# Kernel optimization log

Measured on AMD Instinct MI355X. Metric: run time of the kernel, lower is better.

Reference implementation:

```python
import jax, jax.numpy as jnp
import numpy as np

S, I, CM, C, D, CZ = 128, 512, 256, 32, 32, 128
EPS = 1e-5


def setup_inputs() -> dict:
    key = jax.random.key(0)
    ks = jax.random.split(key, 7)
    x = jax.random.normal(ks[0], (1, S, I, CM), dtype=jnp.float32)
    norm_w = 1.0 + 0.1 * jax.random.normal(ks[1], (CM,), dtype=jnp.float32)
    norm_b = 0.1 * jax.random.normal(ks[2], (CM,), dtype=jnp.float32)
    Wa = jax.random.normal(ks[3], (C, CM), dtype=jnp.float32) / np.sqrt(CM)
    Wb = jax.random.normal(ks[4], (D, CM), dtype=jnp.float32) / np.sqrt(CM)
    Wo = jax.random.normal(ks[5], (CZ, C * D), dtype=jnp.float32) / np.sqrt(C * D)
    bo = 0.1 * jax.random.normal(ks[6], (CZ,), dtype=jnp.float32)
    return {"x": x, "norm_w": norm_w, "norm_b": norm_b, "Wa": Wa, "Wb": Wb, "Wo": Wo, "bo": bo}


def reference(x, norm_w, norm_b, Wa, Wb, Wo, bo):
    m = x[0]                                   # [S, I, CM] (drop leading batch dim)
    mu = jnp.mean(m, axis=-1, keepdims=True)
    var = jnp.mean((m - mu) ** 2, axis=-1, keepdims=True)
    ln = (m - mu) * jax.lax.rsqrt(var + EPS) * norm_w + norm_b
    a = jnp.einsum('sim,cm->sic', ln, Wa)      # [S, I, C]
    b = jnp.einsum('sjm,dm->sjd', ln, Wb)      # [S, J, D]
    s = a.shape[0]
    # outer product mean over S: [I, J, C, D]; flatten order is (c, d) -> c*D + d,
    # matching the reshape(chunk, C, J, D) -> permute(0,2,1,3) -> flatten in the original.
    o = jnp.einsum('sic,sjd->ijcd', a, b) * (1.0 / s)
    z = o.reshape(o.shape[0], o.shape[1], C * D) @ Wo.T + bo  # [I, J, CZ]
    return z[None]                             # [1, I, J, CZ]
```

## Files before the change

kernel.cpp:

```cpp
#include <hip/hip_runtime.h>

#define EPS 1e-5f

typedef _Float16 half8 __attribute__((ext_vector_type(8)));
typedef _Float16 half4 __attribute__((ext_vector_type(4)));
typedef float f32x4 __attribute__((ext_vector_type(4)));

#define AB_STRIDE 72
#define AB_CHUNK  (16384 * AB_STRIDE)

__device__ __forceinline__ void load16_to_lds(const void* g, void* l) {
    __builtin_amdgcn_global_load_lds((__attribute__((address_space(1))) void*)g,
                                     (__attribute__((address_space(3))) void*)l, 16, 0, 0);
}

__global__ void k_cvt(const float* __restrict__ Wo, const float* __restrict__ Wa,
                      const float* __restrict__ Wb, _Float16* __restrict__ WoH,
                      _Float16* __restrict__ WabH)
{
    int t = blockIdx.x * 256 + threadIdx.x;
    if (t < 32768) {
        int n  = t >> 8;
        int k4 = (t & 255) * 4;
        float4 v = *(const float4*)(Wo + (size_t)n * 1024 + k4);
        int c = k4 >> 5, d0 = k4 & 31;
        _Float16* dst = WoH + (size_t)n * 1024 + c;
        dst[(d0 + 0) * 32] = (_Float16)v.x;
        dst[(d0 + 1) * 32] = (_Float16)v.y;
        dst[(d0 + 2) * 32] = (_Float16)v.z;
        dst[(d0 + 3) * 32] = (_Float16)v.w;
    } else {
        int idx = (t - 32768) * 4;
        const float* src = (idx < 8192) ? (Wa + idx) : (Wb + (idx - 8192));
        float4 v = *(const float4*)src;
        half4 h;
        h[0] = (_Float16)v.x; h[1] = (_Float16)v.y; h[2] = (_Float16)v.z; h[3] = (_Float16)v.w;
        *(half4*)(WabH + idx) = h;
    }
}

__global__ __launch_bounds__(512, 4)
void k1_ln_proj(const float* __restrict__ x, const float* __restrict__ nw,
                const float* __restrict__ nb, const _Float16* __restrict__ WabH,
                _Float16* __restrict__ aT, _Float16* __restrict__ bT)
{
    __shared__ _Float16 xln[64 * 264];
    __shared__ _Float16 oT[256 * 40];

    const int tid  = threadIdx.x;
    const int lane = tid & 63;
    const int w    = tid >> 6;
    const int quad = lane >> 4;
    const int l15  = lane & 15;
    const int i0   = (blockIdx.x >> 2) * 4;
    const int sc   = blockIdx.x & 3;

    const int mt  = w & 3;
    const int ntg = w >> 2;

    for (int sub = 0; sub < 2; ++sub) {
        #pragma unroll
        for (int rr = 0; rr < 8; ++rr) {
            int rl = w * 8 + rr;
            int s_ = sc * 32 + sub * 16 + (rl >> 2);
            int i_ = i0 + (rl & 3);
            const float4* xr = (const float4*)(x + ((size_t)s_ * 512 + i_) * 256);
            float4 v = xr[lane];
            float sum = v.x + v.y + v.z + v.w;
            float ss  = v.x * v.x + v.y * v.y + v.z * v.z + v.w * v.w;
            #pragma unroll
            for (int off = 32; off > 0; off >>= 1) {
                sum += __shfl_xor(sum, off);
                ss  += __shfl_xor(ss, off);
            }
            float mu  = sum * (1.f / 256.f);
            float var = ss * (1.f / 256.f) - mu * mu;
            float rs  = rsqrtf(var + EPS);
            float4 gw = ((const float4*)nw)[lane];
            float4 gb = ((const float4*)nb)[lane];
            half4 o;
            o[0] = (_Float16)((v.x - mu) * rs * gw.x + gb.x);
            o[1] = (_Float16)((v.y - mu) * rs * gw.y + gb.y);
            o[2] = (_Float16)((v.z - mu) * rs * gw.z + gb.z);
            o[3] = (_Float16)((v.w - mu) * rs * gw.w + gb.w);
            *(half4*)(xln + rl * 264 + lane * 4) = o;
        }
        __syncthreads();

        f32x4 acc2[2] = {};
        #pragma unroll
        for (int kk = 0; kk < 8; ++kk) {
            half8 af = *(const half8*)(xln + (mt * 16 + l15) * 264 + kk * 32 + quad * 8);
            #pragma unroll
            for (int t = 0; t < 2; ++t) {
                half8 bf = *(const half8*)(WabH + (ntg * 32 + t * 16 + l15) * 256 + kk * 32 + quad * 8);
                acc2[t] = __builtin_amdgcn_mfma_f32_16x16x32_f16(af, bf, acc2[t], 0, 0, 0);
            }
        }

        #pragma unroll
        for (int t = 0; t < 2; ++t) {
            int c64  = ntg * 32 + t * 16 + l15;
            int base = ((c64 >= 32) ? 128 : 0) + (c64 & 31);
            int s_l  = sub * 16 + mt * 4 + quad;
            #pragma unroll
            for (int r = 0; r < 4; ++r)
                oT[(base + r * 32) * 40 + s_l] = (_Float16)acc2[t][r];
        }
        __syncthreads();
    }

    #pragma unroll
    for (int it2 = 0; it2 < 2; ++it2) {
        int u   = it2 * 512 + tid;
        int row = u >> 2;
        int off = (u & 3) * 8;
        half8 v = *(const half8*)(oT + row * 40 + off);
        _Float16* dst = (row < 128) ? aT : bT;
        int grow = i0 * 32 + (row & 127);
        *(half8*)(dst + (size_t)(sc >> 1) * AB_CHUNK + (size_t)grow * 72 + (sc & 1) * 32 + off) = v;
    }
}

__global__ __launch_bounds__(512, 4)
void k2_main(const _Float16* __restrict__ aT, const _Float16* __restrict__ bT,
             const _Float16* __restrict__ WoH, const float* __restrict__ bo,
             float* __restrict__ out)
{
    __shared__ _Float16 smem[33024];
    _Float16* sA = smem;
    _Float16* sB = smem + 256 * AB_STRIDE;
    _Float16* oL = smem;

    const int tid  = threadIdx.x;
    const int lane = tid & 63;
    const int w    = tid >> 6;
    const int quad = lane >> 4;
    const int l15  = lane & 15;
    const int wy   = w >> 1, wx = w & 1;

    const int jt = blockIdx.x, it = blockIdx.y;
    const char* gA = (const char*)(aT + (size_t)it * 256 * AB_STRIDE);
    const char* gB = (const char*)(bT + (size_t)jt * 128 * AB_STRIDE);

    f32x4 acc[4][4] = {};

    for (int ck = 0; ck < 2; ++ck) {
        const char* cA = gA + (size_t)ck * (AB_CHUNK * 2);
        const char* cB = gB + (size_t)ck * (AB_CHUNK * 2);
        for (int seg = w; seg < 54; seg += 8) {
            if (seg < 36) load16_to_lds(cA + seg * 1024 + lane * 16, (char*)sA + seg * 1024 + lane * 16);
            else          load16_to_lds(cB + (seg - 36) * 1024 + lane * 16, (char*)sB + (seg - 36) * 1024 + lane * 16);
        }
        __syncthreads();

        #pragma unroll
        for (int kloc = 0; kloc < 2; ++kloc) {
            half8 af[4], bf[4];
            #pragma unroll
            for (int mt = 0; mt < 4; ++mt)
                af[mt] = *(const half8*)(sA + (wy * 64 + mt * 16 + l15) * AB_STRIDE + kloc * 32 + quad * 8);
            #pragma unroll
            for (int nt = 0; nt < 4; ++nt)
                bf[nt] = *(const half8*)(sB + (wx * 64 + nt * 16 + l15) * AB_STRIDE + kloc * 32 + quad * 8);
            #pragma unroll
            for (int mt = 0; mt < 4; ++mt)
                #pragma unroll
                for (int nt = 0; nt < 4; ++nt)
                    acc[mt][nt] = __builtin_amdgcn_mfma_f32_16x16x32_f16(af[mt], bf[nt], acc[mt][nt], 0, 0, 0);
        }
        __syncthreads();
    }

    #pragma unroll
    for (int mt = 0; mt < 4; ++mt) {
        int c0     = (mt & 1) * 16 + quad * 4;
        int chunk3 = (c0 >> 3);
        int il     = wy * 2 + (mt >> 1);
        #pragma unroll
        for (int nt = 0; nt < 4; ++nt) {
            int d    = (nt & 1) * 16 + l15;
            int jl   = wx * 2 + (nt >> 1);
            int pair = il * 4 + jl;
            int cS   = (c0 & 7) + ((chunk3 ^ ((d >> 1) & 3)) << 3);
            half4 v;
            v[0] = (_Float16)(acc[mt][nt][0] * (1.f / 128.f));
            v[1] = (_Float16)(acc[mt][nt][1] * (1.f / 128.f));
            v[2] = (_Float16)(acc[mt][nt][2] * (1.f / 128.f));
            v[3] = (_Float16)(acc[mt][nt][3] * (1.f / 128.f));
            *(half4*)(oL + pair * 1032 + d * 32 + cS) = v;
        }
    }
    __syncthreads();

    f32x4 zacc[2] = {};
    const int n0 = w * 16 + l15;
    #pragma unroll 4
    for (int kk = 0; kk < 32; ++kk) {
        int csw = (quad ^ ((kk >> 1) & 3)) * 8;
        half8 oa0 = *(const half8*)(oL + (l15) * 1032 + kk * 32 + csw);
        half8 oa1 = *(const half8*)(oL + (16 + l15) * 1032 + kk * 32 + csw);
        half8 w0  = *(const half8*)(WoH + (size_t)n0 * 1024 + kk * 32 + quad * 8);
        zacc[0] = __builtin_amdgcn_mfma_f32_16x16x32_f16(oa0, w0, zacc[0], 0, 0, 0);
        zacc[1] = __builtin_amdgcn_mfma_f32_16x16x32_f16(oa1, w0, zacc[1], 0, 0, 0);
    }

    float bias = bo[w * 16 + l15];
    #pragma unroll
    for (int mt2 = 0; mt2 < 2; ++mt2) {
        #pragma unroll
        for (int r = 0; r < 4; ++r) {
            int il = mt2 * 4 + quad;
            int jl = r;
            out[(((size_t)(it * 8 + il)) * 512 + jt * 4 + jl) * 128 + w * 16 + l15] = zacc[mt2][r] + bias;
        }
    }
}

extern "C" void kernel_launch(void* const* d_in, const int* in_sizes, int n_in,
                              void* d_out, int out_size, void* d_ws, size_t ws_size,
                              hipStream_t stream)
{
    const float* x      = (const float*)d_in[0];
    const float* norm_w = (const float*)d_in[1];
    const float* norm_b = (const float*)d_in[2];
    const float* Wa     = (const float*)d_in[3];
    const float* Wb     = (const float*)d_in[4];
    const float* Wo     = (const float*)d_in[5];
    const float* bo     = (const float*)d_in[6];
    float* out = (float*)d_out;

    _Float16* aT   = (_Float16*)d_ws;
    _Float16* bT   = aT + 2 * (size_t)AB_CHUNK;
    _Float16* WoH  = bT + 2 * (size_t)AB_CHUNK;
    _Float16* WabH = WoH + 131072;

    k_cvt<<<144, 256, 0, stream>>>(Wo, Wa, Wb, WoH, WabH);
    k1_ln_proj<<<512, 512, 0, stream>>>(x, norm_w, norm_b, WabH, aT, bT);
    k2_main<<<dim3(128, 64), 512, 0, stream>>>(aT, bT, WoH, bo, out);
}
```

Before: 475.0 us.

## Software-pipeline LN input loads via async global-to-LDS triple buffer

Result: no change. 481.9 us (+1.5%).

```diff
diff --git a/kernel.cpp b/kernel.cpp
--- a/kernel.cpp
+++ b/kernel.cpp
@@ -44,6 +44,7 @@
                 const float* __restrict__ nb, const _Float16* __restrict__ WabH,
                 _Float16* __restrict__ aT, _Float16* __restrict__ bT)
 {
+    __shared__ float    xraw[3 * 8 * 256];
     __shared__ _Float16 xln[64 * 264];
     __shared__ _Float16 oT[256 * 40];
 
@@ -58,14 +59,27 @@
     const int mt  = w & 3;
     const int ntg = w >> 2;
 
-    for (int sub = 0; sub < 2; ++sub) {
-        #pragma unroll
-        for (int rr = 0; rr < 8; ++rr) {
-            int rl = w * 8 + rr;
-            int s_ = sc * 32 + sub * 16 + (rl >> 2);
-            int i_ = i0 + (rl & 3);
-            const float4* xr = (const float4*)(x + ((size_t)s_ * 512 + i_) * 256);
-            float4 v = xr[lane];
+    const float4 gw = ((const float4*)nw)[lane];
+    const float4 gb = ((const float4*)nb)[lane];
+
+    auto src_of = [&](int c) -> const float* {
+        int rl = ((c & 7) << 3) + w;
+        int s_ = sc * 32 + ((c >> 3) << 4) + (rl >> 2);
+        int i_ = i0 + (rl & 3);
+        return x + ((size_t)s_ * 512 + i_) * 256;
+    };
+
+    load16_to_lds(src_of(0) + lane * 4, xraw + (0 * 8 + w) * 256 + lane * 4);
+    load16_to_lds(src_of(1) + lane * 4, xraw + (1 * 8 + w) * 256 + lane * 4);
+
+    int rb = 0;
+    for (int half = 0; half < 2; ++half) {
+        for (int cc = 0; cc < 8; ++cc) {
+            const int c = half * 8 + cc;
+            if (c == 15) asm volatile("s_waitcnt vmcnt(0)" ::: "memory");
+            else         asm volatile("s_waitcnt vmcnt(1)" ::: "memory");
+
+            const float4 v = *(const float4*)(xraw + (rb * 8 + w) * 256 + lane * 4);
             float sum = v.x + v.y + v.z + v.w;
             float ss  = v.x * v.x + v.y * v.y + v.z * v.z + v.w * v.w;
             #pragma unroll
@@ -76,16 +90,22 @@
             float mu  = sum * (1.f / 256.f);
             float var = ss * (1.f / 256.f) - mu * mu;
             float rs  = rsqrtf(var + EPS);
-            float4 gw = ((const float4*)nw)[lane];
-            float4 gb = ((const float4*)nb)[lane];
             half4 o;
             o[0] = (_Float16)((v.x - mu) * rs * gw.x + gb.x);
             o[1] = (_Float16)((v.y - mu) * rs * gw.y + gb.y);
             o[2] = (_Float16)((v.z - mu) * rs * gw.z + gb.z);
             o[3] = (_Float16)((v.w - mu) * rs * gw.w + gb.w);
+            int rl = (cc << 3) + w;
             *(half4*)(xln + rl * 264 + lane * 4) = o;
-        }
-        __syncthreads();
+
+            if (c + 2 < 16) {
+                int nb3 = rb + 2; if (nb3 >= 3) nb3 -= 3;
+                load16_to_lds(src_of(c + 2) + lane * 4, xraw + (nb3 * 8 + w) * 256 + lane * 4);
+            }
+            ++rb; if (rb == 3) rb = 0;
+        }
+        asm volatile("s_waitcnt lgkmcnt(0)" ::: "memory");
+        __builtin_amdgcn_s_barrier();
 
         f32x4 acc2[2] = {};
         #pragma unroll
@@ -102,12 +122,13 @@
         for (int t = 0; t < 2; ++t) {
             int c64  = ntg * 32 + t * 16 + l15;
             int base = ((c64 >= 32) ? 128 : 0) + (c64 & 31);
-            int s_l  = sub * 16 + mt * 4 + quad;
+            int s_l  = half * 16 + mt * 4 + quad;
             #pragma unroll
             for (int r = 0; r < 4; ++r)
                 oT[(base + r * 32) * 40 + s_l] = (_Float16)acc2[t][r];
         }
-        __syncthreads();
+        asm volatile("s_waitcnt lgkmcnt(0)" ::: "memory");
+        __builtin_amdgcn_s_barrier();
     }
 
     #pragma unroll
```
